# Optimization experiments

Measured on AMD Instinct MI355X. Metric: run time of the kernel, lower is better.

The kernel has to match this reference:

```python
import jax, jax.numpy as jnp
import numpy as np

NUM_CAMS = 4
E = 256          # embed_dim
H_HEADS = 8      # num_heads
DH = E // H_HEADS
CIN = 64
FF = 4 * E
N_LAYERS = 2
EPS = 1e-5


def _layer_norm(x, g, b):
    mu = jnp.mean(x, axis=-1, keepdims=True)
    var = jnp.mean((x - mu) ** 2, axis=-1, keepdims=True)
    return (x - mu) * jax.lax.rsqrt(var + EPS) * g + b


def setup_inputs() -> dict:
    key = jax.random.key(0)
    ks = jax.random.split(key, 20)
    s = 0.02
    inp = {
        "features": jax.random.normal(ks[0], (NUM_CAMS, 2, CIN, 96, 96), jnp.float32),
        # 1x1 input projection conv
        "Wp": jax.random.normal(ks[1], (E, CIN), jnp.float32) * s,
        "bp": jnp.zeros((E,), jnp.float32),
        # per-layer attention params (stacked over 2 layers)
        "Wqkv": jax.random.normal(ks[2], (N_LAYERS, 3 * E, E), jnp.float32) * s,
        "bqkv": jnp.zeros((N_LAYERS, 3 * E), jnp.float32),
        "Wo": jax.random.normal(ks[3], (N_LAYERS, E, E), jnp.float32) * s,
        "bo": jnp.zeros((N_LAYERS, E), jnp.float32),
        # FFN
        "W1": jax.random.normal(ks[4], (N_LAYERS, FF, E), jnp.float32) * s,
        "b1": jnp.zeros((N_LAYERS, FF), jnp.float32),
        "W2": jax.random.normal(ks[5], (N_LAYERS, E, FF), jnp.float32) * s,
        "b2": jnp.zeros((N_LAYERS, E), jnp.float32),
        # LayerNorms
        "g1": jnp.ones((N_LAYERS, E), jnp.float32),
        "be1": jnp.zeros((N_LAYERS, E), jnp.float32),
        "g2": jnp.ones((N_LAYERS, E), jnp.float32),
        "be2": jnp.zeros((N_LAYERS, E), jnp.float32),
        # 1x1 output conv
        "Wout": jax.random.normal(ks[6], (CIN, E), jnp.float32) * s,
        "bout": jnp.zeros((CIN,), jnp.float32),
    }
    return inp


def reference(features, Wp, bp, Wqkv, bqkv, Wo, bo, W1, b1, W2, b2,
              g1, be1, g2, be2, Wout, bout):
    n_cam, B, Cin, Hh, Ww = features.shape
    # 1x1 conv projection + rearrange to per-pixel sequences: [B*H*W, n_cam, E]
    x = jnp.einsum('nbchw,ec->bhwne', features, Wp) + bp
    x = x.reshape(B * Hh * Ww, n_cam, E)

    scale = 1.0 / jnp.sqrt(jnp.float32(DH))
    for i in range(N_LAYERS):
        # self-attention (post-norm encoder layer, dropout=identity in eval)
        qkv = x @ Wqkv[i].T + bqkv[i]                      # [N, S, 3E]
        q, k, v = jnp.split(qkv, 3, axis=-1)
        q = q.reshape(-1, n_cam, H_HEADS, DH)
        k = k.reshape(-1, n_cam, H_HEADS, DH)
        v = v.reshape(-1, n_cam, H_HEADS, DH)
        scores = jnp.einsum('nqhd,nkhd->nhqk', q, k) * scale
        attn = jax.nn.softmax(scores, axis=-1)
        sa = jnp.einsum('nhqk,nkhd->nqhd', attn, v).reshape(-1, n_cam, E)
        sa = sa @ Wo[i].T + bo[i]
        x = _layer_norm(x + sa, g1[i], be1[i])
        # FFN (ReLU activation, default)
        ff = jax.nn.relu(x @ W1[i].T + b1[i]) @ W2[i].T + b2[i]
        x = _layer_norm(x + ff, g2[i], be2[i])

    # mean over cameras, back to [B, C, H, W] via 1x1 output conv
    fused = x.mean(axis=1).reshape(B, Hh, Ww, E)
    out = jnp.einsum('bhwe,ce->bchw', fused, Wout) + bout[None, :, None, None]
    return out
```

## Files before the change

kernel.cpp:

```cpp
#include <hip/hip_runtime.h>
#include <cstdint>
#include <cstddef>


typedef __bf16 bf16;
typedef __bf16 bf16x8 __attribute__((ext_vector_type(8)));
typedef __bf16 bf16x4 __attribute__((ext_vector_type(4)));
typedef float  f32x4  __attribute__((ext_vector_type(4)));

__device__ __forceinline__ void async_copy16(const void* g, void* l)
{
    __builtin_amdgcn_global_load_lds(
        (__attribute__((address_space(1))) void*)g,
        (__attribute__((address_space(3))) void*)l,
        16, 0, 0);
}

__global__ void pack_all_k(const float* __restrict__ s0, const float* __restrict__ s1,
                           const float* __restrict__ s2, const float* __restrict__ s3,
                           const float* __restrict__ s4,
                           bf16* __restrict__ d0, bf16* __restrict__ d1,
                           bf16* __restrict__ d2, bf16* __restrict__ d3,
                           bf16* __restrict__ d4)
{
    const int i = blockIdx.x * 256 + threadIdx.x;
    if (i < 393216)       d0[i] = (bf16)s0[i];
    else if (i < 524288)  d1[i - 393216] = (bf16)s1[i - 393216];
    else if (i < 1048576) d2[i - 524288] = (bf16)s2[i - 524288];
    else if (i < 1572864) d3[i - 1048576] = (bf16)s3[i - 1048576];
    else                  d4[i - 1572864] = (bf16)s4[i - 1572864];
}

__global__ __launch_bounds__(256) void feat_pack_k(const float* __restrict__ feat,
                                                   bf16* __restrict__ Xf)
{
    __shared__ float ft[64][68];

    const int tid  = threadIdx.x;
    const int camb = blockIdx.y;
    const int cam  = camb >> 1;
    const int b    = camb & 1;
    const int hw0  = blockIdx.x * 64;

    const float* fb = feat + (size_t)camb * 64 * 9216 + hw0;
#pragma unroll
    for (int rep = 0; rep < 16; ++rep) {
        const int idx = rep * 256 + tid;
        const int c = idx >> 6, p = idx & 63;
        ft[p][c] = fb[(size_t)c * 9216 + p];
    }
    __syncthreads();

    const int pbase = b * 9216 + hw0;
#pragma unroll
    for (int rep = 0; rep < 2; ++rep) {
        const int idx = rep * 256 + tid;
        const int p = idx >> 3, cc = idx & 7;
        const f32x4 a = *(const f32x4*)(&ft[p][cc * 8]);
        const f32x4 c4 = *(const f32x4*)(&ft[p][cc * 8 + 4]);
        bf16x8 v;
#pragma unroll
        for (int i = 0; i < 4; ++i) { v[i] = (bf16)a[i]; v[4 + i] = (bf16)c4[i]; }
        const size_t t = (size_t)(pbase + p) * 4 + cam;
        *(bf16x8*)(Xf + t * 64 + cc * 8) = v;
    }
}

template <bool RELU>
__global__ __launch_bounds__(256, 2) void gemm_bt(
    const bf16* __restrict__ A, const bf16* __restrict__ B,
    const float* __restrict__ bias, bf16* __restrict__ C,
    int N, int K)
{
    __shared__ __align__(16) bf16 As[128 * 64];
    __shared__ __align__(16) bf16 Bs[128 * 64];

    const int tid  = threadIdx.x;
    const int lane = tid & 63;
    const int wv   = tid >> 6;
    const int wm   = wv >> 1;
    const int wn   = wv & 1;
    const int bm   = blockIdx.y * 128;
    const int bn   = blockIdx.x * 128;

    const int r8  = lane >> 3;
    const int p8  = lane & 7;
    const int gch = p8 ^ r8;

    const int quad = lane >> 4;
    const int l16  = lane & 15;

    f32x4 acc[4][4] = {};

    for (int k0 = 0; k0 < K; k0 += 64) {
#pragma unroll
        for (int inst = 0; inst < 4; ++inst) {
            const int row = wv * 32 + inst * 8 + r8;
            const bf16* ga = A + (size_t)(bm + row) * K + (k0 + gch * 8);
            const bf16* gb = B + (size_t)(bn + row) * K + (k0 + gch * 8);
            async_copy16(ga, (char*)As + (wv * 4 + inst) * 1024);
            async_copy16(gb, (char*)Bs + (wv * 4 + inst) * 1024);
        }
        __syncthreads();

#pragma unroll
        for (int kk = 0; kk < 2; ++kk) {
            bf16x8 af[4], bfr[4];
            const int lch = kk * 4 + quad;
#pragma unroll
            for (int i = 0; i < 4; ++i) {
                const int m = wm * 64 + i * 16 + l16;
                af[i] = *(const bf16x8*)((const char*)As + (m * 8 + (lch ^ (m & 7))) * 16);
                const int n = wn * 64 + i * 16 + l16;
                bfr[i] = *(const bf16x8*)((const char*)Bs + (n * 8 + (lch ^ (n & 7))) * 16);
            }
#pragma unroll
            for (int i = 0; i < 4; ++i)
#pragma unroll
                for (int j = 0; j < 4; ++j)
                    acc[i][j] = __builtin_amdgcn_mfma_f32_16x16x32_bf16(
                        af[i], bfr[j], acc[i][j], 0, 0, 0);
        }
        __syncthreads();
    }

#pragma unroll
    for (int j = 0; j < 4; ++j) {
        const int n = bn + wn * 64 + j * 16 + l16;
        const float bv = bias[n];
#pragma unroll
        for (int i = 0; i < 4; ++i) {
            const int mb = bm + wm * 64 + i * 16 + quad * 4;
#pragma unroll
            for (int r = 0; r < 4; ++r) {
                float v = acc[i][j][r] + bv;
                if (RELU) v = fmaxf(v, 0.f);
                C[(size_t)(mb + r) * N + n] = (bf16)v;
            }
        }
    }
}

__global__ __launch_bounds__(256, 2) void gemm_ln_k(
    const bf16* __restrict__ A, const bf16* __restrict__ B,
    const float* __restrict__ bias, const bf16* __restrict__ Xres,
    const float* __restrict__ gam, const float* __restrict__ bet,
    bf16* __restrict__ Xout, int K)
{
    __shared__ __align__(16) bf16 S[24576];
    __shared__ float2 red[128][2];

    const int tid  = threadIdx.x;
    const int lane = tid & 63;
    const int wv   = tid >> 6;
    const int wm   = wv >> 1;
    const int wn   = wv & 1;
    const int bm   = blockIdx.x * 128;
    const int quad = lane >> 4;
    const int l16  = lane & 15;

    f32x4 acc[4][8] = {};

    for (int k0 = 0; k0 < K; k0 += 64) {
#pragma unroll
        for (int s = 0; s < 12; ++s) {
            const int L   = s * 256 + tid;
            const int row = L >> 3;
            const int gch = (L & 7) ^ (row & 7);
            const bf16* g = (row < 128)
                ? A + (size_t)(bm + row) * K + (k0 + gch * 8)
                : B + (size_t)(row - 128) * K + (k0 + gch * 8);
            async_copy16(g, (char*)S + (size_t)L * 16);
        }
        __syncthreads();

#pragma unroll
        for (int kk = 0; kk < 2; ++kk) {
            const int lch = kk * 4 + quad;
            bf16x8 af[4], bfr[8];
#pragma unroll
            for (int i = 0; i < 4; ++i) {
                const int m = wm * 64 + i * 16 + l16;
                af[i] = *(const bf16x8*)((const char*)S + (m * 8 + (lch ^ (m & 7))) * 16);
            }
#pragma unroll
            for (int j = 0; j < 8; ++j) {
                const int n = wn * 128 + j * 16 + l16;
                bfr[j] = *(const bf16x8*)((const char*)S + ((128 + n) * 8 + (lch ^ (n & 7))) * 16);
            }
#pragma unroll
            for (int i = 0; i < 4; ++i)
#pragma unroll
                for (int j = 0; j < 8; ++j)
                    acc[i][j] = __builtin_amdgcn_mfma_f32_16x16x32_bf16(
                        af[i], bfr[j], acc[i][j], 0, 0, 0);
        }
        __syncthreads();
    }

    float bv[8], gv[8], bev[8];
#pragma unroll
    for (int j = 0; j < 8; ++j) {
        const int n = wn * 128 + j * 16 + l16;
        bv[j] = bias[n]; gv[j] = gam[n]; bev[j] = bet[n];
    }

#pragma unroll
    for (int i = 0; i < 4; ++i) {
#pragma unroll
        for (int r = 0; r < 4; ++r) {
            const int rl  = wm * 64 + i * 16 + quad * 4 + r;
            const size_t row = (size_t)(bm + rl);
            float s1 = 0.f, s2 = 0.f;
#pragma unroll
            for (int j = 0; j < 8; ++j) {
                const int n = wn * 128 + j * 16 + l16;
                const float v = acc[i][j][r] + bv[j] + (float)Xres[row * 256 + n];
                acc[i][j][r] = v;
                s1 += v; s2 += v * v;
            }
#pragma unroll
            for (int off = 1; off < 16; off <<= 1) {
                s1 += __shfl_xor(s1, off, 64);
                s2 += __shfl_xor(s2, off, 64);
            }
            if (l16 == 0) red[rl][wn] = make_float2(s1, s2);
        }
    }
    __syncthreads();

#pragma unroll
    for (int i = 0; i < 4; ++i) {
#pragma unroll
        for (int r = 0; r < 4; ++r) {
            const int rl = wm * 64 + i * 16 + quad * 4 + r;
            const float2 p0 = red[rl][0], p1 = red[rl][1];
            const float mu  = (p0.x + p1.x) * (1.f / 256.f);
            const float ex2 = (p0.y + p1.y) * (1.f / 256.f);
            const float rstd = rsqrtf(fmaxf(ex2 - mu * mu, 0.f) + 1e-5f);
            const size_t row = (size_t)(bm + rl);
#pragma unroll
            for (int j = 0; j < 8; ++j) {
                const int n = wn * 128 + j * 16 + l16;
                Xout[row * 256 + n] = (bf16)((acc[i][j][r] - mu) * rstd * gv[j] + bev[j]);
            }
        }
    }
}

__device__ __forceinline__ void ffn_stage(int s, const bf16* __restrict__ W1,
                                          const bf16* __restrict__ W2,
                                          char* buf, int tid)
{
    const int hc = s >> 3;
    const int q  = s & 7;
    if (q < 4) {
#pragma unroll
        for (int it = 0; it < 4; ++it) {
            const int L = it * 256 + tid;
            const int row = L >> 3, psl = L & 7;
            const int c = psl ^ (row & 7);
            async_copy16(W1 + (size_t)(hc * 128 + row) * 256 + q * 64 + c * 8,
                         buf + (size_t)L * 16);
        }
    } else {
#pragma unroll
        for (int it = 0; it < 4; ++it) {
            const int L = it * 256 + tid;
            const int r128 = L >> 3, psl = L & 7;
            const int g = psl ^ (r128 & 7);
            const int n = r128 * 2 + (g >> 2);
            const int c = g & 3;
            async_copy16(W2 + (size_t)n * 1024 + hc * 128 + (q - 4) * 32 + c * 8,
                         buf + (size_t)L * 16);
        }
    }
}

__global__ __launch_bounds__(256, 2) void ffn_fused_k(
    const bf16* __restrict__ X,
    const bf16* __restrict__ W1, const float* __restrict__ b1,
    const bf16* __restrict__ W2, const float* __restrict__ b2,
    const float* __restrict__ gam, const float* __restrict__ bet,
    bf16* __restrict__ Xout)
{
    __shared__ __align__(16) char smem[81920];
    bf16* Xs = (bf16*)smem;
    bf16* Ts = (bf16*)(smem + 32768);
    float2 (*red)[2] = (float2 (*)[2])(void*)(smem + 32768);
    char* stg = smem + 49152;

    const int tid  = threadIdx.x;
    const int lane = tid & 63;
    const int wv   = tid >> 6;
    const int wm   = wv >> 1;
    const int wn   = wv & 1;
    const int quad = lane >> 4;
    const int l16  = lane & 15;
    const int bm   = blockIdx.x * 64;

#pragma unroll
    for (int it = 0; it < 8; ++it) {
        const int L = it * 256 + tid;
        const int row = L >> 5, slot = L & 31;
        const int gch = (slot & 24) | ((slot ^ row) & 7);
        async_copy16(X + (size_t)(bm + row) * 256 + gch * 8,
                     (char*)Xs + (size_t)L * 16);
    }
    ffn_stage(0, W1, W2, stg, tid);
    __syncthreads();

    f32x4 acc2[2][8] = {};

#pragma unroll 1
    for (int hc = 0; hc < 8; ++hc) {
        f32x4 accA[2][4] = {};

#pragma unroll
        for (int q = 0; q < 4; ++q) {
            const int s = hc * 8 + q;
            const char* cur = stg + (size_t)(s & 1) * 16384;
            ffn_stage(s + 1, W1, W2, stg + (size_t)((s + 1) & 1) * 16384, tid);
#pragma unroll
            for (int kk = 0; kk < 2; ++kk) {
                const int ch = kk * 4 + quad;
                const int gc = q * 8 + ch;
                bf16x8 af[2], bfr[4];
#pragma unroll
                for (int i = 0; i < 2; ++i) {
                    const int m  = wm * 32 + i * 16 + l16;
                    const int sl = (gc & 24) | ((gc ^ m) & 7);
                    af[i] = *(const bf16x8*)((const char*)Xs + (m * 32 + sl) * 16);
                }
#pragma unroll
                for (int j = 0; j < 4; ++j) {
                    const int n  = wn * 64 + j * 16 + l16;
                    const int sl = ch ^ (n & 7);
                    bfr[j] = *(const bf16x8*)(cur + (n * 8 + sl) * 16);
                }
#pragma unroll
                for (int i = 0; i < 2; ++i)
#pragma unroll
                    for (int j = 0; j < 4; ++j)
                        accA[i][j] = __builtin_amdgcn_mfma_f32_16x16x32_bf16(
                            af[i], bfr[j], accA[i][j], 0, 0, 0);
            }
            __syncthreads();
        }

#pragma unroll
        for (int j = 0; j < 4; ++j) {
            const int h  = wn * 64 + j * 16 + l16;
            const float bb = b1[hc * 128 + h];
            const int g  = h >> 3;
#pragma unroll
            for (int i = 0; i < 2; ++i)
#pragma unroll
                for (int r = 0; r < 4; ++r) {
                    const int m  = wm * 32 + i * 16 + quad * 4 + r;
                    const int sl = (g & 8) | ((g ^ m) & 7);
                    const float v = fmaxf(accA[i][j][r] + bb, 0.f);
                    *((bf16*)((char*)Ts + (m * 16 + sl) * 16 + (h & 7) * 2)) = (bf16)v;
                }
        }
        __syncthreads();

#pragma unroll
        for (int q = 0; q < 4; ++q) {
            const int s = hc * 8 + 4 + q;
            const char* cur = stg + (size_t)(s & 1) * 16384;
            if (s < 63)
                ffn_stage(s + 1, W1, W2, stg + (size_t)((s + 1) & 1) * 16384, tid);
            const int tc = q * 4 + quad;
            bf16x8 af[2], bfr[8];
#pragma unroll
            for (int i = 0; i < 2; ++i) {
                const int m  = wm * 32 + i * 16 + l16;
                const int sl = (tc & 8) | ((tc ^ m) & 7);
                af[i] = *(const bf16x8*)((const char*)Ts + (m * 16 + sl) * 16);
            }
#pragma unroll
            for (int j = 0; j < 8; ++j) {
                const int n  = wn * 128 + j * 16 + l16;
                const int sl = (((n & 1) * 4 + quad) ^ ((n >> 1) & 7)) & 7;
                bfr[j] = *(const bf16x8*)(cur + ((n >> 1) * 8 + sl) * 16);
            }
#pragma unroll
            for (int i = 0; i < 2; ++i)
#pragma unroll
                for (int j = 0; j < 8; ++j)
                    acc2[i][j] = __builtin_amdgcn_mfma_f32_16x16x32_bf16(
                        af[i], bfr[j], acc2[i][j], 0, 0, 0);
            __syncthreads();
        }
    }

    float bv[8], gv[8], bev[8];
#pragma unroll
    for (int j = 0; j < 8; ++j) {
        const int n = wn * 128 + j * 16 + l16;
        bv[j] = b2[n]; gv[j] = gam[n]; bev[j] = bet[n];
    }

#pragma unroll
    for (int i = 0; i < 2; ++i) {
#pragma unroll
        for (int r = 0; r < 4; ++r) {
            const int rl = wm * 32 + i * 16 + quad * 4 + r;
            float s1 = 0.f, s2 = 0.f;
#pragma unroll
            for (int j = 0; j < 8; ++j) {
                const int n  = wn * 128 + j * 16 + l16;
                const int gc = n >> 3;
                const int sl = (gc & 24) | ((gc ^ rl) & 7);
                const float xr = (float)*((const bf16*)((const char*)Xs +
                                   (rl * 32 + sl) * 16 + (n & 7) * 2));
                const float v = acc2[i][j][r] + bv[j] + xr;
                acc2[i][j][r] = v;
                s1 += v; s2 += v * v;
            }
#pragma unroll
            for (int off = 1; off < 16; off <<= 1) {
                s1 += __shfl_xor(s1, off, 64);
                s2 += __shfl_xor(s2, off, 64);
            }
            if (l16 == 0) red[rl][wn] = make_float2(s1, s2);
        }
    }
    __syncthreads();

#pragma unroll
    for (int i = 0; i < 2; ++i) {
#pragma unroll
        for (int r = 0; r < 4; ++r) {
            const int rl = wm * 32 + i * 16 + quad * 4 + r;
            const float2 p0 = red[rl][0], p1 = red[rl][1];
            const float mu  = (p0.x + p1.x) * (1.f / 256.f);
            const float ex2 = (p0.y + p1.y) * (1.f / 256.f);
            const float rstd = rsqrtf(fmaxf(ex2 - mu * mu, 0.f) + 1e-5f);
            const size_t row = (size_t)(bm + rl);
#pragma unroll
            for (int j = 0; j < 8; ++j) {
                const int n = wn * 128 + j * 16 + l16;
                Xout[row * 256 + n] = (bf16)((acc2[i][j][r] - mu) * rstd * gv[j] + bev[j]);
            }
        }
    }
}

__global__ __launch_bounds__(256) void attention_k(const bf16* __restrict__ QKV,
                                                   bf16* __restrict__ SA)
{
    __shared__ float qf[4][4][768];
    __shared__ float sc[4][8][4][4];

    const int tid  = threadIdx.x;
    const int wv   = tid >> 6;
    const int lane = tid & 63;
    const int s    = blockIdx.x * 4 + wv;

    const bf16* base = QKV + (size_t)s * 4 * 768;
#pragma unroll
    for (int it = 0; it < 6; ++it) {
        const int idx = it * 64 + lane;
        const bf16x8 v = *(const bf16x8*)(base + idx * 8);
        const int tok = idx / 96;
        const int e   = (idx % 96) * 8;
        f32x4 f0, f1;
#pragma unroll
        for (int i = 0; i < 4; ++i) { f0[i] = (float)v[i]; f1[i] = (float)v[4 + i]; }
        *(f32x4*)(&qf[wv][tok][e])     = f0;
        *(f32x4*)(&qf[wv][tok][e + 4]) = f1;
    }
    __syncthreads();

#pragma unroll
    for (int rep = 0; rep < 2; ++rep) {
        const int t = rep * 64 + lane;
        const int h = t >> 4, i = (t >> 2) & 3, j = t & 3;
        const float* q = &qf[wv][i][h * 32];
        const float* k = &qf[wv][j][256 + h * 32];
        float a = 0.f;
#pragma unroll
        for (int dd = 0; dd < 32; ++dd) {
            const int d = (dd + lane) & 31;
            a += q[d] * k[d];
        }
        sc[wv][h][i][j] = a * 0.17677669529663687f;
    }
    __syncthreads();

    if (lane < 32) {
        const int h = lane >> 2, i = lane & 3;
        float s0 = sc[wv][h][i][0], s1 = sc[wv][h][i][1];
        float s2 = sc[wv][h][i][2], s3 = sc[wv][h][i][3];
        float m = fmaxf(fmaxf(s0, s1), fmaxf(s2, s3));
        float e0 = expf(s0 - m), e1 = expf(s1 - m);
        float e2 = expf(s2 - m), e3 = expf(s3 - m);
        float inv = 1.f / (e0 + e1 + e2 + e3);
        sc[wv][h][i][0] = e0 * inv;
        sc[wv][h][i][1] = e1 * inv;
        sc[wv][h][i][2] = e2 * inv;
        sc[wv][h][i][3] = e3 * inv;
    }
    __syncthreads();

    const int h = lane >> 3;
#pragma unroll
    for (int i = 0; i < 4; ++i) {
        f32x4 a = {0.f, 0.f, 0.f, 0.f};
#pragma unroll
        for (int j = 0; j < 4; ++j) {
            const float p = sc[wv][h][i][j];
            const f32x4 v = *(const f32x4*)(&qf[wv][j][512 + lane * 4]);
#pragma unroll
            for (int q = 0; q < 4; ++q) a[q] += p * v[q];
        }
        bf16x4 o;
#pragma unroll
        for (int q = 0; q < 4; ++q) o[q] = (bf16)a[q];
        *(bf16x4*)(SA + (size_t)(s * 4 + i) * 256 + lane * 4) = o;
    }
}

__global__ __launch_bounds__(256) void out_proj_k(const bf16* __restrict__ X,
                                                  const float* __restrict__ Wout,
                                                  const float* __restrict__ bout,
                                                  float* __restrict__ out)
{
    __shared__ float fused[16][260];
    const int tid = threadIdx.x;
    const int p0  = blockIdx.x * 16;

#pragma unroll
    for (int it = 0; it < 16; ++it) {
        const int idx = it * 256 + tid;
        const int pix = idx >> 8, e = idx & 255;
        const size_t base = (size_t)(p0 + pix) * 1024 + e;
        const float s = (float)X[base] + (float)X[base + 256] +
                        (float)X[base + 512] + (float)X[base + 768];
        fused[pix][e] = s * 0.25f;
    }
    __syncthreads();

    const int pix = tid & 15;
    const int c0  = tid >> 4;
    const int p   = p0 + pix;
    const int b   = p / 9216;
    const int hw  = p % 9216;
#pragma unroll
    for (int it = 0; it < 4; ++it) {
        const int c = it * 16 + c0;
        const float* w = Wout + c * 256;
        float acc = bout[c];
#pragma unroll 8
        for (int e = 0; e < 256; ++e) acc += fused[pix][e] * w[e];
        out[((size_t)b * 64 + c) * 9216 + hw] = acc;
    }
}

extern "C" void kernel_launch(void* const* d_in, const int* in_sizes, int n_in,
                              void* d_out, int out_size, void* d_ws, size_t ws_size,
                              hipStream_t stream)
{
    const float* features = (const float*)d_in[0];
    const float* Wp   = (const float*)d_in[1];
    const float* bp   = (const float*)d_in[2];
    const float* Wqkv = (const float*)d_in[3];
    const float* bqkv = (const float*)d_in[4];
    const float* Wo   = (const float*)d_in[5];
    const float* bo   = (const float*)d_in[6];
    const float* W1   = (const float*)d_in[7];
    const float* b1   = (const float*)d_in[8];
    const float* W2   = (const float*)d_in[9];
    const float* b2   = (const float*)d_in[10];
    const float* g1   = (const float*)d_in[11];
    const float* be1  = (const float*)d_in[12];
    const float* g2   = (const float*)d_in[13];
    const float* be2  = (const float*)d_in[14];
    const float* Wout = (const float*)d_in[15];
    const float* bout = (const float*)d_in[16];
    float* out = (float*)d_out;

    char* ws = (char*)d_ws;
    bf16* X   = (bf16*)(ws);
    bf16* QKV = (bf16*)(ws + 37748736ull);
    bf16* SAb = (bf16*)(ws + 150994944ull);
    bf16* Xf  = (bf16*)(ws + 188743680ull);
    bf16* WpB = (bf16*)(ws + 198180864ull);
    bf16* Wb  = (bf16*)(ws + 226492416ull);

    bf16* WqkvB = Wb;
    bf16* WoB   = Wb + 393216;
    bf16* W1B   = Wb + 524288;
    bf16* W2B   = Wb + 1048576;

    pack_all_k<<<6208, 256, 0, stream>>>(Wqkv, Wo, W1, W2, Wp,
                                         WqkvB, WoB, W1B, W2B, WpB);

    feat_pack_k<<<dim3(144, 8), 256, 0, stream>>>(features, Xf);
    gemm_bt<false><<<dim3(2, 576), 256, 0, stream>>>(Xf, WpB, bp, X, 256, 64);

    for (int l = 0; l < 2; ++l) {
        gemm_bt<false><<<dim3(6, 576), 256, 0, stream>>>(
            X, WqkvB + l * 196608, bqkv + l * 768, QKV, 768, 256);
        attention_k<<<4608, 256, 0, stream>>>(QKV, SAb);
        gemm_ln_k<<<576, 256, 0, stream>>>(
            SAb, WoB + l * 65536, bo + l * 256, X,
            g1 + l * 256, be1 + l * 256, X, 256);
        ffn_fused_k<<<1152, 256, 0, stream>>>(
            X, W1B + l * 262144, b1 + l * 1024,
            W2B + l * 262144, b2 + l * 256,
            g2 + l * 256, be2 + l * 256, X);
    }

    out_proj_k<<<1152, 256, 0, stream>>>(X, Wout, bout, out);
}
```

Before: 648.1 us.

## Stage FFN weights through registers with two-deep prefetch instead of async LDS copies

Replaces the direct global-to-LDS async copies of W1/W2 tiles in the fused FFN kernel with register-staged loads issued two stages ahead and stored to LDS after the MFMA work of the current stage. It also folds the ReLU/bias write of the hidden tile into the last GEMM1 stage, removing one barrier per hidden chunk. The intent is to hide global load latency behind compute with a deeper prefetch. The cost is 32 extra VGPRs of staging registers, which may pressure occupancy under launch_bounds(256,2), plus explicit LDS store instructions.

```diff
diff --git a/kernel.cpp b/kernel.cpp
--- a/kernel.cpp
+++ b/kernel.cpp
@@ -248,9 +248,9 @@
     }
 }
 
-__device__ __forceinline__ void ffn_stage(int s, const bf16* __restrict__ W1,
-                                          const bf16* __restrict__ W2,
-                                          char* buf, int tid)
+__device__ __forceinline__ void ffn_ld(int s, const bf16* __restrict__ W1,
+                                       const bf16* __restrict__ W2,
+                                       int tid, uint4* r)
 {
     const int hc = s >> 3;
     const int q  = s & 7;
@@ -258,23 +258,29 @@
 #pragma unroll
         for (int it = 0; it < 4; ++it) {
             const int L = it * 256 + tid;
-            const int row = L >> 3, psl = L & 7;
-            const int c = psl ^ (row & 7);
-            async_copy16(W1 + (size_t)(hc * 128 + row) * 256 + q * 64 + c * 8,
-                         buf + (size_t)L * 16);
+            const int row = L >> 3;
+            const int c = (L & 7) ^ (row & 7);
+            r[it] = *(const uint4*)(W1 + (size_t)(hc * 128 + row) * 256 + q * 64 + c * 8);
         }
     } else {
 #pragma unroll
         for (int it = 0; it < 4; ++it) {
             const int L = it * 256 + tid;
-            const int r128 = L >> 3, psl = L & 7;
-            const int g = psl ^ (r128 & 7);
+            const int r128 = L >> 3;
+            const int g = (L & 7) ^ (r128 & 7);
             const int n = r128 * 2 + (g >> 2);
             const int c = g & 3;
-            async_copy16(W2 + (size_t)n * 1024 + hc * 128 + (q - 4) * 32 + c * 8,
-                         buf + (size_t)L * 16);
-        }
-    }
+            r[it] = *(const uint4*)(W2 + (size_t)n * 1024 + hc * 128 + (q - 4) * 32 + c * 8);
+        }
+    }
+}
+
+__device__ __forceinline__ void ffn_st(int s, char* stg, int tid, const uint4* r)
+{
+    char* buf = stg + (size_t)(s & 1) * 16384;
+#pragma unroll
+    for (int it = 0; it < 4; ++it)
+        *(uint4*)(buf + (size_t)(it * 256 + tid) * 16) = r[it];
 }
 
 __global__ __launch_bounds__(256, 2) void ffn_fused_k(
@@ -299,6 +305,9 @@
     const int l16  = lane & 15;
     const int bm   = blockIdx.x * 64;
 
+    uint4 rp[2][4];
+
+    ffn_ld(0, W1, W2, tid, rp[0]);
 #pragma unroll
     for (int it = 0; it < 8; ++it) {
         const int L = it * 256 + tid;
@@ -307,7 +316,8 @@
         async_copy16(X + (size_t)(bm + row) * 256 + gch * 8,
                      (char*)Xs + (size_t)L * 16);
     }
-    ffn_stage(0, W1, W2, stg, tid);
+    ffn_st(0, stg, tid, rp[0]);
+    ffn_ld(1, W1, W2, tid, rp[1]);
     __syncthreads();
 
     f32x4 acc2[2][8] = {};
@@ -319,8 +329,8 @@
 #pragma unroll
         for (int q = 0; q < 4; ++q) {
             const int s = hc * 8 + q;
+            ffn_ld(s + 2, W1, W2, tid, rp[s & 1]);
             const char* cur = stg + (size_t)(s & 1) * 16384;
-            ffn_stage(s + 1, W1, W2, stg + (size_t)((s + 1) & 1) * 16384, tid);
 #pragma unroll
             for (int kk = 0; kk < 2; ++kk) {
                 const int ch = kk * 4 + quad;
@@ -345,32 +355,32 @@
                         accA[i][j] = __builtin_amdgcn_mfma_f32_16x16x32_bf16(
                             af[i], bfr[j], accA[i][j], 0, 0, 0);
             }
+            ffn_st(s + 1, stg, tid, rp[(s + 1) & 1]);
+            if (q == 3) {
+#pragma unroll
+                for (int j = 0; j < 4; ++j) {
+                    const int h  = wn * 64 + j * 16 + l16;
+                    const float bb = b1[hc * 128 + h];
+                    const int g  = h >> 3;
+#pragma unroll
+                    for (int i = 0; i < 2; ++i)
+#pragma unroll
+                        for (int r = 0; r < 4; ++r) {
+                            const int m  = wm * 32 + i * 16 + quad * 4 + r;
+                            const int sl = (g & 8) | ((g ^ m) & 7);
+                            const float v = fmaxf(accA[i][j][r] + bb, 0.f);
+                            *((bf16*)((char*)Ts + (m * 16 + sl) * 16 + (h & 7) * 2)) = (bf16)v;
+                        }
+                }
+            }
             __syncthreads();
         }
-
-#pragma unroll
-        for (int j = 0; j < 4; ++j) {
-            const int h  = wn * 64 + j * 16 + l16;
-            const float bb = b1[hc * 128 + h];
-            const int g  = h >> 3;
-#pragma unroll
-            for (int i = 0; i < 2; ++i)
-#pragma unroll
-                for (int r = 0; r < 4; ++r) {
-                    const int m  = wm * 32 + i * 16 + quad * 4 + r;
-                    const int sl = (g & 8) | ((g ^ m) & 7);
-                    const float v = fmaxf(accA[i][j][r] + bb, 0.f);
-                    *((bf16*)((char*)Ts + (m * 16 + sl) * 16 + (h & 7) * 2)) = (bf16)v;
-                }
-        }
-        __syncthreads();
 
 #pragma unroll
         for (int q = 0; q < 4; ++q) {
             const int s = hc * 8 + 4 + q;
+            if (s + 2 < 64) ffn_ld(s + 2, W1, W2, tid, rp[s & 1]);
             const char* cur = stg + (size_t)(s & 1) * 16384;
-            if (s < 63)
-                ffn_stage(s + 1, W1, W2, stg + (size_t)((s + 1) & 1) * 16384, tid);
             const int tc = q * 4 + quad;
             bf16x8 af[2], bfr[8];
 #pragma unroll
@@ -391,6 +401,7 @@
                 for (int j = 0; j < 8; ++j)
                     acc2[i][j] = __builtin_amdgcn_mfma_f32_16x16x32_bf16(
                         af[i], bfr[j], acc2[i][j], 0, 0, 0);
+            if (s + 1 < 64) ffn_st(s + 1, stg, tid, rp[(s + 1) & 1]);
             __syncthreads();
         }
     }
```

Result: slower. 1.277 ms (+97.0%).

## Hold FFN input tile in registers and double weight stage size

Applied to the files above, without the earlier changes.

The fused FFN kernel now loads the 64x256 X tile directly into registers as MFMA A-fragments instead of staging it in LDS. The freed shared memory lets each weight stage double to 32 KB, which halves the number of pipeline stages and __syncthreads barriers per hidden chunk. The residual add in the epilogue now reads X from global memory. This adds register pressure (16 bf16x8 vectors per thread at 2 blocks/CU), which could cause spills or lower occupancy, and it brings in uncoalesced global reads for the residual.

```diff
diff --git a/kernel.cpp b/kernel.cpp
--- a/kernel.cpp
+++ b/kernel.cpp
@@ -248,30 +248,29 @@
     }
 }
 
-__device__ __forceinline__ void ffn_stage(int s, const bf16* __restrict__ W1,
-                                          const bf16* __restrict__ W2,
-                                          char* buf, int tid)
-{
-    const int hc = s >> 3;
-    const int q  = s & 7;
-    if (q < 4) {
-#pragma unroll
-        for (int it = 0; it < 4; ++it) {
+__device__ __forceinline__ void ffn_stage32(int st, const bf16* __restrict__ W1,
+                                            const bf16* __restrict__ W2,
+                                            char* stg, int tid)
+{
+    char* buf = stg + (size_t)(st & 1) * 32768;
+    const int hc = st >> 2;
+    const int ps = st & 3;
+    if (ps < 2) {
+#pragma unroll
+        for (int it = 0; it < 8; ++it) {
             const int L = it * 256 + tid;
-            const int row = L >> 3, psl = L & 7;
-            const int c = psl ^ (row & 7);
-            async_copy16(W1 + (size_t)(hc * 128 + row) * 256 + q * 64 + c * 8,
+            const int row = L >> 4, pslot = L & 15;
+            const int c = (pslot & 8) | ((pslot ^ row) & 7);
+            async_copy16(W1 + (size_t)(hc * 128 + row) * 256 + ps * 128 + c * 8,
                          buf + (size_t)L * 16);
         }
     } else {
 #pragma unroll
-        for (int it = 0; it < 4; ++it) {
+        for (int it = 0; it < 8; ++it) {
             const int L = it * 256 + tid;
-            const int r128 = L >> 3, psl = L & 7;
-            const int g = psl ^ (r128 & 7);
-            const int n = r128 * 2 + (g >> 2);
-            const int c = g & 3;
-            async_copy16(W2 + (size_t)n * 1024 + hc * 128 + (q - 4) * 32 + c * 8,
+            const int row = L >> 3, pslot = L & 7;
+            const int c = pslot ^ (row & 7);
+            async_copy16(W2 + (size_t)row * 1024 + hc * 128 + (ps - 2) * 64 + c * 8,
                          buf + (size_t)L * 16);
         }
     }
@@ -285,10 +284,9 @@
     bf16* __restrict__ Xout)
 {
     __shared__ __align__(16) char smem[81920];
-    bf16* Xs = (bf16*)smem;
-    bf16* Ts = (bf16*)(smem + 32768);
-    float2 (*red)[2] = (float2 (*)[2])(void*)(smem + 32768);
-    char* stg = smem + 49152;
+    bf16* Ts = (bf16*)smem;
+    float2 (*red)[2] = (float2 (*)[2])(void*)smem;
+    char* stg = smem + 16384;
 
     const int tid  = threadIdx.x;
     const int lane = tid & 63;
@@ -299,15 +297,15 @@
     const int l16  = lane & 15;
     const int bm   = blockIdx.x * 64;
 
-#pragma unroll
-    for (int it = 0; it < 8; ++it) {
-        const int L = it * 256 + tid;
-        const int row = L >> 5, slot = L & 31;
-        const int gch = (slot & 24) | ((slot ^ row) & 7);
-        async_copy16(X + (size_t)(bm + row) * 256 + gch * 8,
-                     (char*)Xs + (size_t)L * 16);
-    }
-    ffn_stage(0, W1, W2, stg, tid);
+    bf16x8 xa[2][8];
+#pragma unroll
+    for (int i = 0; i < 2; ++i)
+#pragma unroll
+        for (int c = 0; c < 8; ++c)
+            xa[i][c] = *(const bf16x8*)(X + (size_t)(bm + wm * 32 + i * 16 + l16) * 256
+                                          + c * 32 + quad * 8);
+
+    ffn_stage32(0, W1, W2, stg, tid);
     __syncthreads();
 
     f32x4 acc2[2][8] = {};
@@ -317,80 +315,77 @@
         f32x4 accA[2][4] = {};
 
 #pragma unroll
-        for (int q = 0; q < 4; ++q) {
-            const int s = hc * 8 + q;
-            const char* cur = stg + (size_t)(s & 1) * 16384;
-            ffn_stage(s + 1, W1, W2, stg + (size_t)((s + 1) & 1) * 16384, tid);
+        for (int half = 0; half < 2; ++half) {
+            const int st = hc * 4 + half;
+            ffn_stage32(st + 1, W1, W2, stg, tid);
+            const char* cur = stg + (size_t)(st & 1) * 32768;
+#pragma unroll
+            for (int kk = 0; kk < 4; ++kk) {
+                const int lch = kk * 4 + quad;
+                bf16x8 bfr[4];
+#pragma unroll
+                for (int j = 0; j < 4; ++j) {
+                    const int n  = wn * 64 + j * 16 + l16;
+                    const int sl = (lch & 8) | ((lch ^ n) & 7);
+                    bfr[j] = *(const bf16x8*)(cur + (n * 16 + sl) * 16);
+                }
+#pragma unroll
+                for (int i = 0; i < 2; ++i)
+#pragma unroll
+                    for (int j = 0; j < 4; ++j)
+                        accA[i][j] = __builtin_amdgcn_mfma_f32_16x16x32_bf16(
+                            xa[i][half * 4 + kk], bfr[j], accA[i][j], 0, 0, 0);
+            }
+            if (half == 1) {
+#pragma unroll
+                for (int j = 0; j < 4; ++j) {
+                    const int h  = wn * 64 + j * 16 + l16;
+                    const float bb = b1[hc * 128 + h];
+                    const int g  = h >> 3;
+#pragma unroll
+                    for (int i = 0; i < 2; ++i)
+#pragma unroll
+                        for (int r = 0; r < 4; ++r) {
+                            const int m  = wm * 32 + i * 16 + quad * 4 + r;
+                            const int sl = (g & 8) | ((g ^ m) & 7);
+                            const float v = fmaxf(accA[i][j][r] + bb, 0.f);
+                            *((bf16*)((char*)Ts + (m * 16 + sl) * 16 + (h & 7) * 2)) = (bf16)v;
+                        }
+                }
+            }
+            __syncthreads();
+        }
+
+#pragma unroll
+        for (int half = 0; half < 2; ++half) {
+            const int st = hc * 4 + 2 + half;
+            if (st + 1 < 32) ffn_stage32(st + 1, W1, W2, stg, tid);
+            const char* cur = stg + (size_t)(st & 1) * 32768;
 #pragma unroll
             for (int kk = 0; kk < 2; ++kk) {
-                const int ch = kk * 4 + quad;
-                const int gc = q * 8 + ch;
-                bf16x8 af[2], bfr[4];
+                const int tcg = half * 8 + kk * 4 + quad;
+                bf16x8 af[2];
 #pragma unroll
                 for (int i = 0; i < 2; ++i) {
                     const int m  = wm * 32 + i * 16 + l16;
-                    const int sl = (gc & 24) | ((gc ^ m) & 7);
-                    af[i] = *(const bf16x8*)((const char*)Xs + (m * 32 + sl) * 16);
+                    const int sl = (tcg & 8) | ((tcg ^ m) & 7);
+                    af[i] = *(const bf16x8*)((const char*)Ts + (m * 16 + sl) * 16);
                 }
-#pragma unroll
-                for (int j = 0; j < 4; ++j) {
-                    const int n  = wn * 64 + j * 16 + l16;
-                    const int sl = ch ^ (n & 7);
+                bf16x8 bfr[8];
+#pragma unroll
+                for (int j = 0; j < 8; ++j) {
+                    const int n  = wn * 128 + j * 16 + l16;
+                    const int tl = kk * 4 + quad;
+                    const int sl = tl ^ (n & 7);
                     bfr[j] = *(const bf16x8*)(cur + (n * 8 + sl) * 16);
                 }
 #pragma unroll
                 for (int i = 0; i < 2; ++i)
 #pragma unroll
-                    for (int j = 0; j < 4; ++j)
-                        accA[i][j] = __builtin_amdgcn_mfma_f32_16x16x32_bf16(
-                            af[i], bfr[j], accA[i][j], 0, 0, 0);
-            }
-            __syncthreads();
-        }
-
-#pragma unroll
-        for (int j = 0; j < 4; ++j) {
-            const int h  = wn * 64 + j * 16 + l16;
-            const float bb = b1[hc * 128 + h];
-            const int g  = h >> 3;
-#pragma unroll
-            for (int i = 0; i < 2; ++i)
-#pragma unroll
-                for (int r = 0; r < 4; ++r) {
-                    const int m  = wm * 32 + i * 16 + quad * 4 + r;
-                    const int sl = (g & 8) | ((g ^ m) & 7);
-                    const float v = fmaxf(accA[i][j][r] + bb, 0.f);
-                    *((bf16*)((char*)Ts + (m * 16 + sl) * 16 + (h & 7) * 2)) = (bf16)v;
-                }
-        }
-        __syncthreads();
-
-#pragma unroll
-        for (int q = 0; q < 4; ++q) {
-            const int s = hc * 8 + 4 + q;
-            const char* cur = stg + (size_t)(s & 1) * 16384;
-            if (s < 63)
-                ffn_stage(s + 1, W1, W2, stg + (size_t)((s + 1) & 1) * 16384, tid);
-            const int tc = q * 4 + quad;
-            bf16x8 af[2], bfr[8];
-#pragma unroll
-            for (int i = 0; i < 2; ++i) {
-                const int m  = wm * 32 + i * 16 + l16;
-                const int sl = (tc & 8) | ((tc ^ m) & 7);
-                af[i] = *(const bf16x8*)((const char*)Ts + (m * 16 + sl) * 16);
-            }
-#pragma unroll
-            for (int j = 0; j < 8; ++j) {
-                const int n  = wn * 128 + j * 16 + l16;
-                const int sl = (((n & 1) * 4 + quad) ^ ((n >> 1) & 7)) & 7;
-                bfr[j] = *(const bf16x8*)(cur + ((n >> 1) * 8 + sl) * 16);
-            }
-#pragma unroll
-            for (int i = 0; i < 2; ++i)
-#pragma unroll
-                for (int j = 0; j < 8; ++j)
-                    acc2[i][j] = __builtin_amdgcn_mfma_f32_16x16x32_bf16(
-                        af[i], bfr[j], acc2[i][j], 0, 0, 0);
+                    for (int j = 0; j < 8; ++j)
+                        acc2[i][j] = __builtin_amdgcn_mfma_f32_16x16x32_bf16(
+                            af[i], bfr[j], acc2[i][j], 0, 0, 0);
+            }
             __syncthreads();
         }
     }
@@ -407,15 +402,12 @@
 #pragma unroll
         for (int r = 0; r < 4; ++r) {
             const int rl = wm * 32 + i * 16 + quad * 4 + r;
+            const size_t row = (size_t)(bm + rl);
             float s1 = 0.f, s2 = 0.f;
 #pragma unroll
             for (int j = 0; j < 8; ++j) {
-                const int n  = wn * 128 + j * 16 + l16;
-                const int gc = n >> 3;
-                const int sl = (gc & 24) | ((gc ^ rl) & 7);
-                const float xr = (float)*((const bf16*)((const char*)Xs +
-                                   (rl * 32 + sl) * 16 + (n & 7) * 2));
-                const float v = acc2[i][j][r] + bv[j] + xr;
+                const int n = wn * 128 + j * 16 + l16;
+                const float v = acc2[i][j][r] + bv[j] + (float)X[row * 256 + n];
                 acc2[i][j][r] = v;
                 s1 += v; s2 += v * v;
             }
```

Result: slower. 848.6 us (+30.9%).

## Pre-swizzle weights into MFMA fragment layout and read B directly from global

Applied to the files above, without the earlier changes.

Weights are now packed once into a per-lane MFMA fragment order, so each GEMM kernel loads B operands straight from global/L2 as contiguous 16-byte vectors instead of staging them through LDS. The A tile is loaded into LDS in full once, which removes the per-k-step barriers and the FFN double-buffered weight staging. This cuts LDS traffic, synchronisation and shared memory use (FFN drops to 48KB, which may allow more blocks per CU). The trade-off is that weight reads now depend on L2/global latency inside the MFMA loop, with no software prefetch.

```diff
diff --git a/kernel.cpp b/kernel.cpp
--- a/kernel.cpp
+++ b/kernel.cpp
@@ -16,19 +16,36 @@
         16, 0, 0);
 }
 
-__global__ void pack_all_k(const float* __restrict__ s0, const float* __restrict__ s1,
-                           const float* __restrict__ s2, const float* __restrict__ s3,
-                           const float* __restrict__ s4,
-                           bf16* __restrict__ d0, bf16* __restrict__ d1,
-                           bf16* __restrict__ d2, bf16* __restrict__ d3,
-                           bf16* __restrict__ d4)
-{
-    const int i = blockIdx.x * 256 + threadIdx.x;
-    if (i < 393216)       d0[i] = (bf16)s0[i];
-    else if (i < 524288)  d1[i - 393216] = (bf16)s1[i - 393216];
-    else if (i < 1048576) d2[i - 524288] = (bf16)s2[i - 524288];
-    else if (i < 1572864) d3[i - 1048576] = (bf16)s3[i - 1048576];
-    else                  d4[i - 1572864] = (bf16)s4[i - 1572864];
+__global__ void pack_frag_k(const float* __restrict__ Wp, const float* __restrict__ Wqkv,
+                            const float* __restrict__ Wo, const float* __restrict__ W1,
+                            const float* __restrict__ W2,
+                            bf16* __restrict__ WpF, bf16* __restrict__ WqkvF,
+                            bf16* __restrict__ WoF, bf16* __restrict__ W1F,
+                            bf16* __restrict__ W2F)
+{
+    const int g = blockIdx.x * 256 + threadIdx.x;
+    const float* src; bf16* dst; int K, e;
+    if (g < 2048)        { src = Wp;  dst = WpF;  K = 64;  e = g; }
+    else if (g < 51200)  { int r = g - 2048;  int l = r / 24576; e = r % 24576;
+                           src = Wqkv + l * 196608; dst = WqkvF + l * 196608; K = 256; }
+    else if (g < 67584)  { int r = g - 51200; int l = r / 8192;  e = r % 8192;
+                           src = Wo + l * 65536;   dst = WoF + l * 65536;   K = 256; }
+    else if (g < 133120) { int r = g - 67584; int l = r / 32768; e = r % 32768;
+                           src = W1 + l * 262144;  dst = W1F + l * 262144;  K = 256; }
+    else                 { int r = g - 133120; int l = r / 32768; e = r % 32768;
+                           src = W2 + l * 262144;  dst = W2F + l * 262144;  K = 1024; }
+
+    const int perNT = (K >> 5) << 6;
+    const int nt   = e / perNT;
+    const int rem  = e % perNT;
+    const int kc   = rem >> 6;
+    const int lane = rem & 63;
+    const int row  = nt * 16 + (lane & 15);
+    const int col  = kc * 32 + (lane >> 4) * 8;
+    bf16x8 v;
+#pragma unroll
+    for (int q = 0; q < 8; ++q) v[q] = (bf16)src[(size_t)row * K + col + q];
+    *(bf16x8*)(dst + (size_t)e * 8) = v;
 }
 
 __global__ __launch_bounds__(256) void feat_pack_k(const float* __restrict__ feat,
@@ -66,14 +83,13 @@
     }
 }
 
-template <bool RELU>
-__global__ __launch_bounds__(256, 2) void gemm_bt(
-    const bf16* __restrict__ A, const bf16* __restrict__ B,
-    const float* __restrict__ bias, bf16* __restrict__ C,
-    int N, int K)
-{
-    __shared__ __align__(16) bf16 As[128 * 64];
-    __shared__ __align__(16) bf16 Bs[128 * 64];
+template <int K, bool RELU>
+__global__ __launch_bounds__(256, 2) void gemm_a(
+    const bf16* __restrict__ A, const bf16* __restrict__ Bf,
+    const float* __restrict__ bias, bf16* __restrict__ C, int Ntot)
+{
+    __shared__ __align__(16) char As[128 * K * 2];
+    constexpr int CPR = K / 8;
 
     const int tid  = threadIdx.x;
     const int lane = tid & 63;
@@ -82,46 +98,42 @@
     const int wn   = wv & 1;
     const int bm   = blockIdx.y * 128;
     const int bn   = blockIdx.x * 128;
-
-    const int r8  = lane >> 3;
-    const int p8  = lane & 7;
-    const int gch = p8 ^ r8;
-
+    const int nt0  = blockIdx.x * 8;
     const int quad = lane >> 4;
     const int l16  = lane & 15;
 
+#pragma unroll
+    for (int it = 0; it < K / 16; ++it) {
+        const int L = it * 256 + tid;
+        const int row = L / CPR, s = L % CPR;
+        const int c = (s & ~7) | ((s ^ row) & 7);
+        async_copy16(A + (size_t)(bm + row) * K + c * 8, As + (size_t)L * 16);
+    }
+    __syncthreads();
+
     f32x4 acc[4][4] = {};
 
-    for (int k0 = 0; k0 < K; k0 += 64) {
-#pragma unroll
-        for (int inst = 0; inst < 4; ++inst) {
-            const int row = wv * 32 + inst * 8 + r8;
-            const bf16* ga = A + (size_t)(bm + row) * K + (k0 + gch * 8);
-            const bf16* gb = B + (size_t)(bn + row) * K + (k0 + gch * 8);
-            async_copy16(ga, (char*)As + (wv * 4 + inst) * 1024);
-            async_copy16(gb, (char*)Bs + (wv * 4 + inst) * 1024);
-        }
-        __syncthreads();
-
-#pragma unroll
-        for (int kk = 0; kk < 2; ++kk) {
-            bf16x8 af[4], bfr[4];
-            const int lch = kk * 4 + quad;
-#pragma unroll
-            for (int i = 0; i < 4; ++i) {
-                const int m = wm * 64 + i * 16 + l16;
-                af[i] = *(const bf16x8*)((const char*)As + (m * 8 + (lch ^ (m & 7))) * 16);
-                const int n = wn * 64 + i * 16 + l16;
-                bfr[i] = *(const bf16x8*)((const char*)Bs + (n * 8 + (lch ^ (n & 7))) * 16);
-            }
-#pragma unroll
-            for (int i = 0; i < 4; ++i)
-#pragma unroll
-                for (int j = 0; j < 4; ++j)
-                    acc[i][j] = __builtin_amdgcn_mfma_f32_16x16x32_bf16(
-                        af[i], bfr[j], acc[i][j], 0, 0, 0);
-        }
-        __syncthreads();
+#pragma unroll
+    for (int kk = 0; kk < K / 32; ++kk) {
+        bf16x8 af[4], bfr[4];
+        const int gc = kk * 4 + quad;
+#pragma unroll
+        for (int i = 0; i < 4; ++i) {
+            const int m  = wm * 64 + i * 16 + l16;
+            const int sl = (gc & ~7) | ((gc ^ m) & 7);
+            af[i] = *(const bf16x8*)(As + (size_t)(m * CPR + sl) * 16);
+        }
+#pragma unroll
+        for (int j = 0; j < 4; ++j) {
+            const int nt = nt0 + wn * 4 + j;
+            bfr[j] = *(const bf16x8*)(Bf + ((size_t)(nt * (K / 32) + kk) * 64 + lane) * 8);
+        }
+#pragma unroll
+        for (int i = 0; i < 4; ++i)
+#pragma unroll
+            for (int j = 0; j < 4; ++j)
+                acc[i][j] = __builtin_amdgcn_mfma_f32_16x16x32_bf16(
+                    af[i], bfr[j], acc[i][j], 0, 0, 0);
     }
 
 #pragma unroll
@@ -135,19 +147,19 @@
             for (int r = 0; r < 4; ++r) {
                 float v = acc[i][j][r] + bv;
                 if (RELU) v = fmaxf(v, 0.f);
-                C[(size_t)(mb + r) * N + n] = (bf16)v;
-            }
-        }
-    }
-}
-
-__global__ __launch_bounds__(256, 2) void gemm_ln_k(
-    const bf16* __restrict__ A, const bf16* __restrict__ B,
+                C[(size_t)(mb + r) * Ntot + n] = (bf16)v;
+            }
+        }
+    }
+}
+
+__global__ __launch_bounds__(256, 2) void gemm_ln_a(
+    const bf16* __restrict__ A, const bf16* __restrict__ Bf,
     const float* __restrict__ bias, const bf16* __restrict__ Xres,
     const float* __restrict__ gam, const float* __restrict__ bet,
-    bf16* __restrict__ Xout, int K)
-{
-    __shared__ __align__(16) bf16 S[24576];
+    bf16* __restrict__ Xout)
+{
+    __shared__ __align__(16) char As[128 * 256 * 2];
     __shared__ float2 red[128][2];
 
     const int tid  = threadIdx.x;
@@ -159,43 +171,38 @@
     const int quad = lane >> 4;
     const int l16  = lane & 15;
 
+#pragma unroll
+    for (int it = 0; it < 16; ++it) {
+        const int L = it * 256 + tid;
+        const int row = L >> 5, s = L & 31;
+        const int c = (s & 24) | ((s ^ row) & 7);
+        async_copy16(A + (size_t)(bm + row) * 256 + c * 8, As + (size_t)L * 16);
+    }
+    __syncthreads();
+
     f32x4 acc[4][8] = {};
 
-    for (int k0 = 0; k0 < K; k0 += 64) {
-#pragma unroll
-        for (int s = 0; s < 12; ++s) {
-            const int L   = s * 256 + tid;
-            const int row = L >> 3;
-            const int gch = (L & 7) ^ (row & 7);
-            const bf16* g = (row < 128)
-                ? A + (size_t)(bm + row) * K + (k0 + gch * 8)
-                : B + (size_t)(row - 128) * K + (k0 + gch * 8);
-            async_copy16(g, (char*)S + (size_t)L * 16);
-        }
-        __syncthreads();
-
-#pragma unroll
-        for (int kk = 0; kk < 2; ++kk) {
-            const int lch = kk * 4 + quad;
-            bf16x8 af[4], bfr[8];
-#pragma unroll
-            for (int i = 0; i < 4; ++i) {
-                const int m = wm * 64 + i * 16 + l16;
-                af[i] = *(const bf16x8*)((const char*)S + (m * 8 + (lch ^ (m & 7))) * 16);
-            }
-#pragma unroll
-            for (int j = 0; j < 8; ++j) {
-                const int n = wn * 128 + j * 16 + l16;
-                bfr[j] = *(const bf16x8*)((const char*)S + ((128 + n) * 8 + (lch ^ (n & 7))) * 16);
-            }
-#pragma unroll
-            for (int i = 0; i < 4; ++i)
-#pragma unroll
-                for (int j = 0; j < 8; ++j)
-                    acc[i][j] = __builtin_amdgcn_mfma_f32_16x16x32_bf16(
-                        af[i], bfr[j], acc[i][j], 0, 0, 0);
-        }
-        __syncthreads();
+#pragma unroll
+    for (int kk = 0; kk < 8; ++kk) {
+        bf16x8 af[4], bfr[8];
+        const int gc = kk * 4 + quad;
+#pragma unroll
+        for (int i = 0; i < 4; ++i) {
+            const int m  = wm * 64 + i * 16 + l16;
+            const int sl = (gc & 24) | ((gc ^ m) & 7);
+            af[i] = *(const bf16x8*)(As + (size_t)(m * 32 + sl) * 16);
+        }
+#pragma unroll
+        for (int j = 0; j < 8; ++j) {
+            const int nt = wn * 8 + j;
+            bfr[j] = *(const bf16x8*)(Bf + ((size_t)(nt * 8 + kk) * 64 + lane) * 8);
+        }
+#pragma unroll
+        for (int i = 0; i < 4; ++i)
+#pragma unroll
+            for (int j = 0; j < 8; ++j)
+                acc[i][j] = __builtin_amdgcn_mfma_f32_16x16x32_bf16(
+                    af[i], bfr[j], acc[i][j], 0, 0, 0);
     }
 
     float bv[8], gv[8], bev[8];
@@ -248,47 +255,17 @@
     }
 }
 
-__device__ __forceinline__ void ffn_stage(int s, const bf16* __restrict__ W1,
-                                          const bf16* __restrict__ W2,
-                                          char* buf, int tid)
-{
-    const int hc = s >> 3;
-    const int q  = s & 7;
-    if (q < 4) {
-#pragma unroll
-        for (int it = 0; it < 4; ++it) {
-            const int L = it * 256 + tid;
-            const int row = L >> 3, psl = L & 7;
-            const int c = psl ^ (row & 7);
-            async_copy16(W1 + (size_t)(hc * 128 + row) * 256 + q * 64 + c * 8,
-                         buf + (size_t)L * 16);
-        }
-    } else {
-#pragma unroll
-        for (int it = 0; it < 4; ++it) {
-            const int L = it * 256 + tid;
-            const int r128 = L >> 3, psl = L & 7;
-            const int g = psl ^ (r128 & 7);
-            const int n = r128 * 2 + (g >> 2);
-            const int c = g & 3;
-            async_copy16(W2 + (size_t)n * 1024 + hc * 128 + (q - 4) * 32 + c * 8,
-                         buf + (size_t)L * 16);
-        }
-    }
-}
-
 __global__ __launch_bounds__(256, 2) void ffn_fused_k(
     const bf16* __restrict__ X,
-    const bf16* __restrict__ W1, const float* __restrict__ b1,
-    const bf16* __restrict__ W2, const float* __restrict__ b2,
+    const bf16* __restrict__ W1f, const float* __restrict__ b1,
+    const bf16* __restrict__ W2f, const float* __restrict__ b2,
     const float* __restrict__ gam, const float* __restrict__ bet,
     bf16* __restrict__ Xout)
 {
-    __shared__ __align__(16) char smem[81920];
+    __shared__ __align__(16) char smem[49152];
     bf16* Xs = (bf16*)smem;
     bf16* Ts = (bf16*)(smem + 32768);
     float2 (*red)[2] = (float2 (*)[2])(void*)(smem + 32768);
-    char* stg = smem + 49152;
 
     const int tid  = threadIdx.x;
     const int lane = tid & 63;
@@ -307,7 +284,6 @@
         async_copy16(X + (size_t)(bm + row) * 256 + gch * 8,
                      (char*)Xs + (size_t)L * 16);
     }
-    ffn_stage(0, W1, W2, stg, tid);
     __syncthreads();
 
     f32x4 acc2[2][8] = {};
@@ -317,36 +293,29 @@
         f32x4 accA[2][4] = {};
 
 #pragma unroll
-        for (int q = 0; q < 4; ++q) {
-            const int s = hc * 8 + q;
-            const char* cur = stg + (size_t)(s & 1) * 16384;
-            ffn_stage(s + 1, W1, W2, stg + (size_t)((s + 1) & 1) * 16384, tid);
-#pragma unroll
-            for (int kk = 0; kk < 2; ++kk) {
-                const int ch = kk * 4 + quad;
-                const int gc = q * 8 + ch;
-                bf16x8 af[2], bfr[4];
-#pragma unroll
-                for (int i = 0; i < 2; ++i) {
-                    const int m  = wm * 32 + i * 16 + l16;
-                    const int sl = (gc & 24) | ((gc ^ m) & 7);
-                    af[i] = *(const bf16x8*)((const char*)Xs + (m * 32 + sl) * 16);
-                }
-#pragma unroll
-                for (int j = 0; j < 4; ++j) {
-                    const int n  = wn * 64 + j * 16 + l16;
-                    const int sl = ch ^ (n & 7);
-                    bfr[j] = *(const bf16x8*)(cur + (n * 8 + sl) * 16);
-                }
-#pragma unroll
-                for (int i = 0; i < 2; ++i)
-#pragma unroll
-                    for (int j = 0; j < 4; ++j)
-                        accA[i][j] = __builtin_amdgcn_mfma_f32_16x16x32_bf16(
-                            af[i], bfr[j], accA[i][j], 0, 0, 0);
-            }
-            __syncthreads();
-        }
+        for (int kk = 0; kk < 8; ++kk) {
+            bf16x8 af[2], bfr[4];
+            const int gc = kk * 4 + quad;
+#pragma unroll
+            for (int i = 0; i < 2; ++i) {
+                const int m  = wm * 32 + i * 16 + l16;
+                const int sl = (gc & 24) | ((gc ^ m) & 7);
+                af[i] = *(const bf16x8*)((const char*)Xs + (m * 32 + sl) * 16);
+            }
+#pragma unroll
+            for (int j = 0; j < 4; ++j) {
+                const int nt = hc * 8 + wn * 4 + j;
+                bfr[j] = *(const bf16x8*)(W1f + ((size_t)(nt * 8 + kk) * 64 + lane) * 8);
+            }
+#pragma unroll
+            for (int i = 0; i < 2; ++i)
+#pragma unroll
+                for (int j = 0; j < 4; ++j)
+                    accA[i][j] = __builtin_amdgcn_mfma_f32_16x16x32_bf16(
+                        af[i], bfr[j], accA[i][j], 0, 0, 0);
+        }
+
+        __syncthreads();
 
 #pragma unroll
         for (int j = 0; j < 4; ++j) {
@@ -366,24 +335,20 @@
         __syncthreads();
 
 #pragma unroll
-        for (int q = 0; q < 4; ++q) {
-            const int s = hc * 8 + 4 + q;
-            const char* cur = stg + (size_t)(s & 1) * 16384;
-            if (s < 63)
-                ffn_stage(s + 1, W1, W2, stg + (size_t)((s + 1) & 1) * 16384, tid);
-            const int tc = q * 4 + quad;
+        for (int kc = 0; kc < 4; ++kc) {
             bf16x8 af[2], bfr[8];
+            const int tc = kc * 4 + quad;
 #pragma unroll
             for (int i = 0; i < 2; ++i) {
                 const int m  = wm * 32 + i * 16 + l16;
                 const int sl = (tc & 8) | ((tc ^ m) & 7);
                 af[i] = *(const bf16x8*)((const char*)Ts + (m * 16 + sl) * 16);
             }
+            const int kcg = hc * 4 + kc;
 #pragma unroll
             for (int j = 0; j < 8; ++j) {
-                const int n  = wn * 128 + j * 16 + l16;
-                const int sl = (((n & 1) * 4 + quad) ^ ((n >> 1) & 7)) & 7;
-                bfr[j] = *(const bf16x8*)(cur + ((n >> 1) * 8 + sl) * 16);
+                const int nt = wn * 8 + j;
+                bfr[j] = *(const bf16x8*)(W2f + ((size_t)(nt * 32 + kcg) * 64 + lane) * 8);
             }
 #pragma unroll
             for (int i = 0; i < 2; ++i)
@@ -391,9 +356,10 @@
                 for (int j = 0; j < 8; ++j)
                     acc2[i][j] = __builtin_amdgcn_mfma_f32_16x16x32_bf16(
                         af[i], bfr[j], acc2[i][j], 0, 0, 0);
-            __syncthreads();
-        }
-    }
+        }
+    }
+
+    __syncthreads();
 
     float bv[8], gv[8], bev[8];
 #pragma unroll
@@ -587,30 +553,30 @@
     bf16* QKV = (bf16*)(ws + 37748736ull);
     bf16* SAb = (bf16*)(ws + 150994944ull);
     bf16* Xf  = (bf16*)(ws + 188743680ull);
-    bf16* WpB = (bf16*)(ws + 198180864ull);
-    bf16* Wb  = (bf16*)(ws + 226492416ull);
-
-    bf16* WqkvB = Wb;
-    bf16* WoB   = Wb + 393216;
-    bf16* W1B   = Wb + 524288;
-    bf16* W2B   = Wb + 1048576;
-
-    pack_all_k<<<6208, 256, 0, stream>>>(Wqkv, Wo, W1, W2, Wp,
-                                         WqkvB, WoB, W1B, W2B, WpB);
+    bf16* WpF = (bf16*)(ws + 198180864ull);
+    bf16* Wfr = (bf16*)(ws + 226492416ull);
+
+    bf16* WqkvF = Wfr;
+    bf16* WoF   = Wfr + 393216;
+    bf16* W1F   = Wfr + 524288;
+    bf16* W2F   = Wfr + 1048576;
+
+    pack_frag_k<<<776, 256, 0, stream>>>(Wp, Wqkv, Wo, W1, W2,
+                                         WpF, WqkvF, WoF, W1F, W2F);
 
     feat_pack_k<<<dim3(144, 8), 256, 0, stream>>>(features, Xf);
-    gemm_bt<false><<<dim3(2, 576), 256, 0, stream>>>(Xf, WpB, bp, X, 256, 64);
+    gemm_a<64, false><<<dim3(2, 576), 256, 0, stream>>>(Xf, WpF, bp, X, 256);
 
     for (int l = 0; l < 2; ++l) {
-        gemm_bt<false><<<dim3(6, 576), 256, 0, stream>>>(
-            X, WqkvB + l * 196608, bqkv + l * 768, QKV, 768, 256);
+        gemm_a<256, false><<<dim3(6, 576), 256, 0, stream>>>(
+            X, WqkvF + l * 196608, bqkv + l * 768, QKV, 768);
         attention_k<<<4608, 256, 0, stream>>>(QKV, SAb);
-        gemm_ln_k<<<576, 256, 0, stream>>>(
-            SAb, WoB + l * 65536, bo + l * 256, X,
-            g1 + l * 256, be1 + l * 256, X, 256);
+        gemm_ln_a<<<576, 256, 0, stream>>>(
+            SAb, WoF + l * 65536, bo + l * 256, X,
+            g1 + l * 256, be1 + l * 256, X);
         ffn_fused_k<<<1152, 256, 0, stream>>>(
-            X, W1B + l * 262144, b1 + l * 1024,
-            W2B + l * 262144, b2 + l * 256,
+            X, W1F + l * 262144, b1 + l * 1024,
+            W2F + l * 262144, b2 + l * 256,
             g2 + l * 256, be2 + l * 256, X);
     }
 
```

Measured after the change: 847.5 us. 1.31x slower.
